# Kernel tuning notes

Measured on AMD Instinct MI355X. Metric: run time of the kernel, lower is better.

The kernel has to match this reference:

```python
import jax, jax.numpy as jnp
import numpy as np

N = 500000      # active voxels
C_IN = 16       # input voxel feature dim
# encoder channels per stage: 32, 64, 128


def setup_inputs() -> dict:
    key = jax.random.key(0)
    ks = jax.random.split(key, 16)

    def w(k, i, o):
        return jax.random.normal(k, (i, o), dtype=jnp.float32) * (1.0 / np.sqrt(i))

    d = {}
    d['feat'] = jax.random.normal(ks[0], (N, C_IN), dtype=jnp.float32)
    d['coords'] = jax.random.randint(ks[1], (N, 4), 0, 1024, dtype=jnp.int32)
    d['W_in'] = w(ks[2], C_IN, 32)
    d['W_enc1'] = w(ks[3], 32, 32)
    d['W_enc2'] = w(ks[4], 32, 64)
    d['W_enc3'] = w(ks[5], 64, 128)
    d['W_lat1'] = w(ks[6], 32, 32)
    d['W_lat2'] = w(ks[7], 64, 64)
    d['W_lat3'] = w(ks[8], 128, 128)
    d['W_merge1'] = w(ks[9], 64, 32)    # merge: 2*C_i -> C_i
    d['W_merge2'] = w(ks[10], 128, 64)
    d['W_merge3'] = w(ks[11], 256, 128)
    d['W_up1'] = w(ks[12], 32, 32)      # upsample: C_i -> C_{i-1}
    d['W_up2'] = w(ks[13], 64, 32)
    d['W_up3'] = w(ks[14], 128, 64)
    return d


def _forward(feat, W_in, W_enc1, W_enc2, W_enc3, W_lat1, W_lat2, W_lat3,
             W_merge1, W_merge2, W_merge3, W_up1, W_up2, W_up3):
    relu = jax.nn.relu
    # conv_input + encoder (1x1 submanifold sparse convs == per-voxel matmul)
    x = relu(feat @ W_in)
    e1 = relu(x @ W_enc1)
    e2 = relu(e1 @ W_enc2)
    e3 = relu(e2 @ W_enc3)
    enc = [e1, e2, e3]
    lats = [W_lat1, W_lat2, W_lat3]
    mrgs = [W_merge1, W_merge2, W_merge3]
    ups = [W_up1, W_up2, W_up3]
    x = e3
    for i in (2, 1, 0):  # decoder stages stage_num..1
        lat = relu(enc[i] @ lats[i])                    # lateral_layer
        # cat0(x_bottom) + cat1(lat): identity-placement 1x1 convs == concat
        cat = jnp.concatenate([x, lat], axis=-1)        # [N, 2*C_i]
        merge = relu(cat @ mrgs[i])                     # merge_layer 2C->C
        red = cat.reshape(cat.shape[0], -1, 2).sum(-1)  # reduce_channel: fixed pairwise-sum conv
        x = relu((merge + red) @ ups[i])                # residual add + upsample_layer
    return x  # ret['voxel_feats']


def reference(feat, coords, W_in, W_enc1, W_enc2, W_enc3, W_lat1, W_lat2, W_lat3,
              W_merge1, W_merge2, W_merge3, W_up1, W_up2, W_up3):
    # coords define sparse structure; for 1x1 subm convs the math only touches features
    return _forward(feat, W_in, W_enc1, W_enc2, W_enc3, W_lat1, W_lat2, W_lat3,
                    W_merge1, W_merge2, W_merge3, W_up1, W_up2, W_up3)
```

## Files before the change

### kernel.cpp

```cpp
#include <hip/hip_runtime.h>

typedef unsigned short u16;
typedef unsigned int u32;
typedef _Float16 h16;
typedef __attribute__((ext_vector_type(2))) _Float16 half2v;
typedef __attribute__((ext_vector_type(8))) _Float16 half8;
typedef __attribute__((ext_vector_type(8))) unsigned short ushort8;
typedef __attribute__((ext_vector_type(4))) float f32x4;
typedef __attribute__((ext_vector_type(16))) float f32x16;

#define NPAIRS 15625
#define STRIPH 12032

#define AE1 0
#define SE1 40
#define AE2 1280
#define SE2 72
#define ACT 3584
#define SCT 264
#define AMR 3712
#define SMR 264

#define MFMA32(A,B,C) __builtin_amdgcn_mfma_f32_32x32x16_f16(A,B,C,0,0,0)

#define LBAR() asm volatile("s_waitcnt lgkmcnt(0)\n\ts_barrier" ::: "memory")
#define LWAIT() asm volatile("s_waitcnt lgkmcnt(0)" ::: "memory")

#define F_L0   0
#define F_L1   1
#define F_L2   3
#define F_L3   7
#define F_L4   23
#define F_L5   55
#define F_L6   119
#define F_L7   135
#define F_L8   143
#define F_L9   159
#define F_L10  163
#define F_L11  165
#define F_L12  169
#define NFRAG  171

__device__ __forceinline__ u16 hb(h16 h) { union { h16 h; u16 u; } v; v.h = h; return v.u; }

__global__ __launch_bounds__(256) void pack_w(
    const float* w0, const float* w1, const float* w2, const float* w3, const float* w4,
    const float* w5, const float* w6, const float* w7, const float* w8, const float* w9,
    const float* w10, const float* w11, const float* w12, u16* __restrict__ packed)
{
  const float* ws[13] = {w0,w1,w2,w3,w4,w5,w6,w7,w8,w9,w10,w11,w12};
  const int Ka[13]  = {16,32,32,64,128,256,128,64,128,64,32,64,32};
  const int KS[13]  = {1,2,2,4,8,16,8,4,8,4,2,4,2};
  const int CO[13]  = {32,32,64,128,128,128,64,64,64,32,32,32,32};
  const int FO[13]  = {F_L0,F_L1,F_L2,F_L3,F_L4,F_L5,F_L6,F_L7,F_L8,F_L9,F_L10,F_L11,F_L12};
  int g = blockIdx.x * 256 + threadIdx.x;
  int f = g >> 6, lane = g & 63;
  if (f >= NFRAG) return;
  int layer = 0;
#pragma unroll
  for (int i = 1; i < 13; ++i) if (f >= FO[i]) layer = i;
  int fl = f - FO[layer];
  int ks = fl % KS[layer];
  int ct = fl / KS[layer];
  int cout = CO[layer];
  int col  = ct * 32 + (lane & 31);
  u16 thi[8], tlo[8];
#pragma unroll
  for (int j = 0; j < 8; ++j) {
    int k = ks * 16 + (lane >> 5) * 8 + j;
    float w = (k < Ka[layer]) ? ws[layer][k * cout + col] : 0.f;
    h16 h = (h16)w;
    h16 l = (h16)(w - (float)h);
    thi[j] = hb(h); tlo[j] = hb(l);
  }
  u16* dst = packed + ((size_t)f * 64 + lane) * 16;
  *(ushort8*)dst       = *(const ushort8*)thi;
  *(ushort8*)(dst + 8) = *(const ushort8*)tlo;
}


__device__ __forceinline__ void splitw(h16* dst, int idx, int dlo, float v) {
  h16 h = (h16)v;
  dst[idx]       = h;
  dst[idx + dlo] = (h16)(v - (float)h);
}

__device__ __forceinline__ float red2p(const h16* catS, int cs, int r16, int cc) {
  half2v hp = *reinterpret_cast<const half2v*>(catS + r16 * cs + 2 * cc);
  half2v lp = *reinterpret_cast<const half2v*>(catS + (r16 + 16) * cs + 2 * cc);
  return (float)hp.x + (float)hp.y + (float)lp.x + (float)lp.y;
}

template<int KS_, int EPI, int BAR>
__device__ __forceinline__ void layer32(
    const h16* __restrict__ asrc, int as,
    const h16* __restrict__ wp, int foff, int ct, int lane,
    half8 pbh, half8 pbl,
    h16* dst, int ds, int colb, const h16* cat, int cs,
    float* __restrict__ gout, int row0)
{
  const int ra = lane & 31;
  const int abase = (ra >> 4) * STRIPH + (ra & 15) * as + ((lane >> 5) << 3);
  const int alo = 16 * as;
  f32x16 acc = {0.f,0.f,0.f,0.f,0.f,0.f,0.f,0.f,0.f,0.f,0.f,0.f,0.f,0.f,0.f,0.f};
#pragma unroll
  for (int ks = 0; ks < KS_; ++ks) {
    half8 bhv, blv;
    if (ks == 0) { bhv = pbh; blv = pbl; }
    else {
      const h16* fp = wp + (((size_t)(foff + ct * KS_ + ks)) * 64 + lane) * 16;
      bhv = *(const half8*)fp;
      blv = *(const half8*)(fp + 8);
    }
    const h16* p = asrc + abase + ks * 16;
    half8 ah = *(const half8*)p;
    half8 al = *(const half8*)(p + alo);
    acc = MFMA32(al, bhv, acc);
    acc = MFMA32(ah, blv, acc);
    acc = MFMA32(ah, bhv, acc);
  }
  const int cc  = ct * 32 + (lane & 31);
  const int hl4 = (lane >> 5) << 2;
  float vr[16];
#pragma unroll
  for (int i = 0; i < 16; ++i) {
    const int rr = (i & 3) + ((i >> 2) << 3) + hl4;
    float v = acc[i] > 0.f ? acc[i] : 0.f;
    if (EPI == 1)
      v += red2p(cat + (rr >> 4) * STRIPH, cs, rr & 15, cc);
    vr[i] = v;
  }
  if (BAR) LBAR();
  if (EPI <= 1) {
    const int dlo = 16 * ds;
#pragma unroll
    for (int i = 0; i < 16; ++i) {
      const int rr = (i & 3) + ((i >> 2) << 3) + hl4;
      splitw(dst + (rr >> 4) * STRIPH, (rr & 15) * ds + colb + cc, dlo, vr[i]);
    }
  } else {
#pragma unroll
    for (int i = 0; i < 16; ++i) {
      const int rr = (i & 3) + ((i >> 2) << 3) + hl4;
      gout[(size_t)(row0 + rr) * 32 + cc] = vr[i];
    }
  }
}

#define PFB(FOFF, CIDX, KS_)                                                        \
  do { const h16* _fp = wp + (((size_t)((FOFF) + (CIDX) * (KS_))) * 64 + lane) * 16; \
       pbh = *(const half8*)_fp; pbl = *(const half8*)(_fp + 8); } while (0)

__global__ __launch_bounds__(256, 3) void backbone(
    const float* __restrict__ feat, const h16* __restrict__ wp, float* __restrict__ out)
{
  __shared__ h16 lds[2 * STRIPH];
  const int lane = threadIdx.x & 63;
  const int wv   = threadIdx.x >> 6;
  const int row0 = blockIdx.x * 32;

  h16* E1 = lds + AE1;
  h16* E2 = lds + AE2;
  h16* CT = lds + ACT;
  h16* MR = lds + AMR;

  half8 pbh, pbl;

  if (wv == 0) {
    PFB(F_L0, 0, 1);
    const int ra = lane & 31;
    const float* sp = feat + (size_t)(row0 + ra) * 16 + ((lane >> 5) << 3);
    f32x4 ua = *(const f32x4*)sp, ub = *(const f32x4*)(sp + 4);
    h16 th[8], tl[8];
#pragma unroll
    for (int j = 0; j < 4; ++j) {
      h16 h;
      h = (h16)ua[j]; th[j]   = h; tl[j]   = (h16)(ua[j] - (float)h);
      h = (h16)ub[j]; th[4+j] = h; tl[4+j] = (h16)(ub[j] - (float)h);
    }
    half8 ah = *(const half8*)th, al = *(const half8*)tl;
    f32x16 a = {0.f,0.f,0.f,0.f,0.f,0.f,0.f,0.f,0.f,0.f,0.f,0.f,0.f,0.f,0.f,0.f};
    a = MFMA32(al, pbh, a); a = MFMA32(ah, pbl, a); a = MFMA32(ah, pbh, a);
    const int cl = lane & 31, hl4 = (lane >> 5) << 2;
    const int dlo = 16 * SCT;
#pragma unroll
    for (int i = 0; i < 16; ++i) {
      const int rr = (i & 3) + ((i >> 2) << 3) + hl4;
      splitw(CT + (rr >> 4) * STRIPH, (rr & 15) * SCT + cl, dlo, a[i] > 0.f ? a[i] : 0.f);
    }
    PFB(F_L1, 0, 2);
    LWAIT();
    layer32<2,0,0>(CT, SCT, wp, F_L1, 0, lane, pbh, pbl, E1, SE1, 0, nullptr, 0, nullptr, 0);
    PFB(F_L2, 0, 2);
  } else if (wv == 1) {
    PFB(F_L2, 1, 2);
  }
  LBAR();

  if (wv < 2) {
    layer32<2,0,0>(E1, SE1, wp, F_L2, wv, lane, pbh, pbl, E2, SE2, 0, nullptr, 0, nullptr, 0);
  }
  PFB(F_L3, wv, 4);
  LBAR();

  layer32<4,0,0>(E2, SE2, wp, F_L3, wv, lane, pbh, pbl, CT, SCT, 0, nullptr, 0, nullptr, 0);
  PFB(F_L4, wv, 8);
  LBAR();

  layer32<8,0,0>(CT, SCT, wp, F_L4, wv, lane, pbh, pbl, CT, SCT, 128, nullptr, 0, nullptr, 0);
  PFB(F_L5, wv, 16);
  LBAR();

  layer32<16,1,1>(CT, SCT, wp, F_L5, wv, lane, pbh, pbl, MR, SMR, 0, CT, SCT, nullptr, 0);
  if (wv < 2) PFB(F_L6, wv, 8); else PFB(F_L7, wv - 2, 4);
  LBAR();

  if (wv < 2) {
    layer32<8,0,0>(MR, SMR, wp, F_L6, wv, lane, pbh, pbl, CT, SCT, 0, nullptr, 0, nullptr, 0);
    PFB(F_L8, wv, 8);
  } else {
    layer32<4,0,0>(E2, SE2, wp, F_L7, wv - 2, lane, pbh, pbl, CT, SCT, 64, nullptr, 0, nullptr, 0);
  }
  LBAR();

  if (wv < 2) {
    layer32<8,1,0>(CT, SCT, wp, F_L8, wv, lane, pbh, pbl, MR, SMR, 0, CT, SCT, nullptr, 0);
  }
  if (wv == 0) PFB(F_L9, 0, 4);
  else if (wv == 1) PFB(F_L10, 0, 2);
  LBAR();

  if (wv == 0) {
    layer32<4,0,0>(MR, SMR, wp, F_L9, 0, lane, pbh, pbl, CT, SCT, 0, nullptr, 0, nullptr, 0);
    PFB(F_L11, 0, 4);
  } else if (wv == 1) {
    layer32<2,0,0>(E1, SE1, wp, F_L10, 0, lane, pbh, pbl, CT, SCT, 32, nullptr, 0, nullptr, 0);
  }
  LBAR();

  if (wv == 0) {
    layer32<4,1,0>(CT, SCT, wp, F_L11, 0, lane, pbh, pbl, MR, SMR, 0, CT, SCT, nullptr, 0);
    PFB(F_L12, 0, 2);
    LWAIT();
    layer32<2,2,0>(MR, SMR, wp, F_L12, 0, lane, pbh, pbl, nullptr, 0, 0, nullptr, 0, out, row0);
  }
}

extern "C" void kernel_launch(void* const* d_in, const int* in_sizes, int n_in,
                              void* d_out, int out_size, void* d_ws, size_t ws_size,
                              hipStream_t stream) {
  (void)in_sizes; (void)n_in; (void)out_size; (void)ws_size;
  u16* packed = (u16*)d_ws;

  hipLaunchKernelGGL(pack_w, dim3(43), dim3(256), 0, stream,
      (const float*)d_in[2],  (const float*)d_in[3],  (const float*)d_in[4],
      (const float*)d_in[5],  (const float*)d_in[8],  (const float*)d_in[11],
      (const float*)d_in[14], (const float*)d_in[7],  (const float*)d_in[10],
      (const float*)d_in[13], (const float*)d_in[6],  (const float*)d_in[9],
      (const float*)d_in[12], packed);

  hipLaunchKernelGGL(backbone, dim3(NPAIRS), dim3(256), 0, stream,
                     (const float*)d_in[0], (const h16*)packed, (float*)d_out);
}
```

Baseline: 456.0 us.

## Prefetch four weight fragments per chunk and split MFMA chain into two accumulators

Weight fragments are now prefetched four k-steps at a time: the first four before the barrier, and later chunks of four are loaded while the current chunk's MFMAs run. This replaces the single-fragment prefetch that left later k-steps waiting on global loads. The MFMA chain is also split across two accumulators, so the hi*hi product no longer depends on the correction products and the dependency chain is shorter. The cost is much higher VGPR pressure (four prefetched fragment pairs plus a second 16-float accumulator), which may hurt occupancy under launch_bounds(256,3) or cause spills. The two accumulators are summed in the epilogue.

```diff
diff --git a/kernel.cpp b/kernel.cpp
--- a/kernel.cpp
+++ b/kernel.cpp
@@ -79,6 +79,27 @@
 }
 
 
+struct fragp { half8 h, l; };
+
+#define LOADFP(DST, BIDX)                                                       \
+  do { const h16* _fp = wp + (((size_t)(BIDX)) * 64 + lane) * 16;               \
+       (DST).h = *(const half8*)_fp; (DST).l = *(const half8*)(_fp + 8); } while (0)
+
+#define PFC(FOFF, CIDX, KS_)                                                    \
+  do { const int _fb = (FOFF) + (CIDX) * (KS_);                                 \
+       LOADFP(pf0, _fb);                                                        \
+       if ((KS_) > 1) LOADFP(pf1, _fb + 1);                                     \
+       if ((KS_) > 2) LOADFP(pf2, _fb + 2);                                     \
+       if ((KS_) > 3) LOADFP(pf3, _fb + 3); } while (0)
+
+#define KSTEP(BP, KSI)                                                          \
+  do { const h16* _p = asrc + abase + (KSI) * 16;                               \
+       half8 _ah = *(const half8*)_p;                                           \
+       half8 _al = *(const half8*)(_p + alo);                                   \
+       accB = MFMA32(_al, (BP).h, accB);                                        \
+       accA = MFMA32(_ah, (BP).h, accA);                                        \
+       accB = MFMA32(_ah, (BP).l, accB); } while (0)
+
 __device__ __forceinline__ void splitw(h16* dst, int idx, int dlo, float v) {
   h16 h = (h16)v;
   dst[idx]       = h;
@@ -95,29 +116,32 @@
 __device__ __forceinline__ void layer32(
     const h16* __restrict__ asrc, int as,
     const h16* __restrict__ wp, int foff, int ct, int lane,
-    half8 pbh, half8 pbl,
+    fragp pf0, fragp pf1, fragp pf2, fragp pf3,
     h16* dst, int ds, int colb, const h16* cat, int cs,
     float* __restrict__ gout, int row0)
 {
   const int ra = lane & 31;
   const int abase = (ra >> 4) * STRIPH + (ra & 15) * as + ((lane >> 5) << 3);
   const int alo = 16 * as;
-  f32x16 acc = {0.f,0.f,0.f,0.f,0.f,0.f,0.f,0.f,0.f,0.f,0.f,0.f,0.f,0.f,0.f,0.f};
-#pragma unroll
-  for (int ks = 0; ks < KS_; ++ks) {
-    half8 bhv, blv;
-    if (ks == 0) { bhv = pbh; blv = pbl; }
-    else {
-      const h16* fp = wp + (((size_t)(foff + ct * KS_ + ks)) * 64 + lane) * 16;
-      bhv = *(const half8*)fp;
-      blv = *(const half8*)(fp + 8);
-    }
-    const h16* p = asrc + abase + ks * 16;
-    half8 ah = *(const half8*)p;
-    half8 al = *(const half8*)(p + alo);
-    acc = MFMA32(al, bhv, acc);
-    acc = MFMA32(ah, blv, acc);
-    acc = MFMA32(ah, bhv, acc);
+  const int fb = foff + ct * KS_;
+  f32x16 accA = {0.f,0.f,0.f,0.f,0.f,0.f,0.f,0.f,0.f,0.f,0.f,0.f,0.f,0.f,0.f,0.f};
+  f32x16 accB = {0.f,0.f,0.f,0.f,0.f,0.f,0.f,0.f,0.f,0.f,0.f,0.f,0.f,0.f,0.f,0.f};
+  fragp cur0 = pf0, cur1 = pf1, cur2 = pf2, cur3 = pf3;
+  constexpr int NCH = (KS_ + 3) / 4;
+#pragma unroll
+  for (int ch = 0; ch < NCH; ++ch) {
+    fragp nx0, nx1, nx2, nx3;
+    if (ch + 1 < NCH) {
+      const int nb = fb + (ch + 1) * 4;
+      LOADFP(nx0, nb + 0); LOADFP(nx1, nb + 1);
+      LOADFP(nx2, nb + 2); LOADFP(nx3, nb + 3);
+    }
+    const int k0 = ch * 4;
+    if (k0 + 0 < KS_) KSTEP(cur0, k0 + 0);
+    if (k0 + 1 < KS_) KSTEP(cur1, k0 + 1);
+    if (k0 + 2 < KS_) KSTEP(cur2, k0 + 2);
+    if (k0 + 3 < KS_) KSTEP(cur3, k0 + 3);
+    if (ch + 1 < NCH) { cur0 = nx0; cur1 = nx1; cur2 = nx2; cur3 = nx3; }
   }
   const int cc  = ct * 32 + (lane & 31);
   const int hl4 = (lane >> 5) << 2;
@@ -125,7 +149,8 @@
 #pragma unroll
   for (int i = 0; i < 16; ++i) {
     const int rr = (i & 3) + ((i >> 2) << 3) + hl4;
-    float v = acc[i] > 0.f ? acc[i] : 0.f;
+    float v = accA[i] + accB[i];
+    v = v > 0.f ? v : 0.f;
     if (EPI == 1)
       v += red2p(cat + (rr >> 4) * STRIPH, cs, rr & 15, cc);
     vr[i] = v;
@@ -146,10 +171,6 @@
     }
   }
 }
-
-#define PFB(FOFF, CIDX, KS_)                                                        \
-  do { const h16* _fp = wp + (((size_t)((FOFF) + (CIDX) * (KS_))) * 64 + lane) * 16; \
-       pbh = *(const half8*)_fp; pbl = *(const half8*)(_fp + 8); } while (0)
 
 __global__ __launch_bounds__(256, 3) void backbone(
     const float* __restrict__ feat, const h16* __restrict__ wp, float* __restrict__ out)
@@ -164,10 +185,10 @@
   h16* CT = lds + ACT;
   h16* MR = lds + AMR;
 
-  half8 pbh, pbl;
+  fragp pf0{}, pf1{}, pf2{}, pf3{};
 
   if (wv == 0) {
-    PFB(F_L0, 0, 1);
+    PFC(F_L0, 0, 1);
     const int ra = lane & 31;
     const float* sp = feat + (size_t)(row0 + ra) * 16 + ((lane >> 5) << 3);
     f32x4 ua = *(const f32x4*)sp, ub = *(const f32x4*)(sp + 4);
@@ -180,7 +201,7 @@
     }
     half8 ah = *(const half8*)th, al = *(const half8*)tl;
     f32x16 a = {0.f,0.f,0.f,0.f,0.f,0.f,0.f,0.f,0.f,0.f,0.f,0.f,0.f,0.f,0.f,0.f};
-    a = MFMA32(al, pbh, a); a = MFMA32(ah, pbl, a); a = MFMA32(ah, pbh, a);
+    a = MFMA32(al, pf0.h, a); a = MFMA32(ah, pf0.l, a); a = MFMA32(ah, pf0.h, a);
     const int cl = lane & 31, hl4 = (lane >> 5) << 2;
     const int dlo = 16 * SCT;
 #pragma unroll
@@ -188,61 +209,73 @@
       const int rr = (i & 3) + ((i >> 2) << 3) + hl4;
       splitw(CT + (rr >> 4) * STRIPH, (rr & 15) * SCT + cl, dlo, a[i] > 0.f ? a[i] : 0.f);
     }
-    PFB(F_L1, 0, 2);
+    PFC(F_L1, 0, 2);
     LWAIT();
-    layer32<2,0,0>(CT, SCT, wp, F_L1, 0, lane, pbh, pbl, E1, SE1, 0, nullptr, 0, nullptr, 0);
-    PFB(F_L2, 0, 2);
+    layer32<2,0,0>(CT, SCT, wp, F_L1, 0, lane, pf0,pf1,pf2,pf3,
+                   E1, SE1, 0, nullptr, 0, nullptr, 0);
+    PFC(F_L2, 0, 2);
   } else if (wv == 1) {
-    PFB(F_L2, 1, 2);
+    PFC(F_L2, 1, 2);
   }
   LBAR();
 
   if (wv < 2) {
-    layer32<2,0,0>(E1, SE1, wp, F_L2, wv, lane, pbh, pbl, E2, SE2, 0, nullptr, 0, nullptr, 0);
-  }
-  PFB(F_L3, wv, 4);
-  LBAR();
-
-  layer32<4,0,0>(E2, SE2, wp, F_L3, wv, lane, pbh, pbl, CT, SCT, 0, nullptr, 0, nullptr, 0);
-  PFB(F_L4, wv, 8);
-  LBAR();
-
-  layer32<8,0,0>(CT, SCT, wp, F_L4, wv, lane, pbh, pbl, CT, SCT, 128, nullptr, 0, nullptr, 0);
-  PFB(F_L5, wv, 16);
-  LBAR();
-
-  layer32<16,1,1>(CT, SCT, wp, F_L5, wv, lane, pbh, pbl, MR, SMR, 0, CT, SCT, nullptr, 0);
-  if (wv < 2) PFB(F_L6, wv, 8); else PFB(F_L7, wv - 2, 4);
+    layer32<2,0,0>(E1, SE1, wp, F_L2, wv, lane, pf0,pf1,pf2,pf3,
+                   E2, SE2, 0, nullptr, 0, nullptr, 0);
+  }
+  PFC(F_L3, wv, 4);
+  LBAR();
+
+  layer32<4,0,0>(E2, SE2, wp, F_L3, wv, lane, pf0,pf1,pf2,pf3,
+                 CT, SCT, 0, nullptr, 0, nullptr, 0);
+  PFC(F_L4, wv, 8);
+  LBAR();
+
+  layer32<8,0,0>(CT, SCT, wp, F_L4, wv, lane, pf0,pf1,pf2,pf3,
+                 CT, SCT, 128, nullptr, 0, nullptr, 0);
+  PFC(F_L5, wv, 16);
+  LBAR();
+
+  layer32<16,1,1>(CT, SCT, wp, F_L5, wv, lane, pf0,pf1,pf2,pf3,
+                  MR, SMR, 0, CT, SCT, nullptr, 0);
+  if (wv < 2) PFC(F_L6, wv, 8); else PFC(F_L7, wv - 2, 4);
   LBAR();
 
   if (wv < 2) {
-    layer32<8,0,0>(MR, SMR, wp, F_L6, wv, lane, pbh, pbl, CT, SCT, 0, nullptr, 0, nullptr, 0);
-    PFB(F_L8, wv, 8);
+    layer32<8,0,0>(MR, SMR, wp, F_L6, wv, lane, pf0,pf1,pf2,pf3,
+                   CT, SCT, 0, nullptr, 0, nullptr, 0);
+    PFC(F_L8, wv, 8);
   } else {
-    layer32<4,0,0>(E2, SE2, wp, F_L7, wv - 2, lane, pbh, pbl, CT, SCT, 64, nullptr, 0, nullptr, 0);
+    layer32<4,0,0>(E2, SE2, wp, F_L7, wv - 2, lane, pf0,pf1,pf2,pf3,
+                   CT, SCT, 64, nullptr, 0, nullptr, 0);
   }
   LBAR();
 
   if (wv < 2) {
-    layer32<8,1,0>(CT, SCT, wp, F_L8, wv, lane, pbh, pbl, MR, SMR, 0, CT, SCT, nullptr, 0);
-  }
-  if (wv == 0) PFB(F_L9, 0, 4);
-  else if (wv == 1) PFB(F_L10, 0, 2);
+    layer32<8,1,0>(CT, SCT, wp, F_L8, wv, lane, pf0,pf1,pf2,pf3,
+                   MR, SMR, 0, CT, SCT, nullptr, 0);
+  }
+  if (wv == 0) PFC(F_L9, 0, 4);
+  else if (wv == 1) PFC(F_L10, 0, 2);
   LBAR();
 
   if (wv == 0) {
-    layer32<4,0,0>(MR, SMR, wp, F_L9, 0, lane, pbh, pbl, CT, SCT, 0, nullptr, 0, nullptr, 0);
-    PFB(F_L11, 0, 4);
+    layer32<4,0,0>(MR, SMR, wp, F_L9, 0, lane, pf0,pf1,pf2,pf3,
+                   CT, SCT, 0, nullptr, 0, nullptr, 0);
+    PFC(F_L11, 0, 4);
   } else if (wv == 1) {
-    layer32<2,0,0>(E1, SE1, wp, F_L10, 0, lane, pbh, pbl, CT, SCT, 32, nullptr, 0, nullptr, 0);
+    layer32<2,0,0>(E1, SE1, wp, F_L10, 0, lane, pf0,pf1,pf2,pf3,
+                   CT, SCT, 32, nullptr, 0, nullptr, 0);
   }
   LBAR();
 
   if (wv == 0) {
-    layer32<4,1,0>(CT, SCT, wp, F_L11, 0, lane, pbh, pbl, MR, SMR, 0, CT, SCT, nullptr, 0);
-    PFB(F_L12, 0, 2);
+    layer32<4,1,0>(CT, SCT, wp, F_L11, 0, lane, pf0,pf1,pf2,pf3,
+                   MR, SMR, 0, CT, SCT, nullptr, 0);
+    PFC(F_L12, 0, 2);
     LWAIT();
-    layer32<2,2,0>(MR, SMR, wp, F_L12, 0, lane, pbh, pbl, nullptr, 0, 0, nullptr, 0, out, row0);
+    layer32<2,2,0>(MR, SMR, wp, F_L12, 0, lane, pf0,pf1,pf2,pf3,
+                   nullptr, 0, 0, nullptr, 0, out, row0);
   }
 }
 
```

Measured after the change: 441.1 us. 1.03x faster.
